# Kernel optimization log

Hardware: AMD Instinct MI355X
Metric: run time of the kernel (lower is better)

## Reference

```python
import jax, jax.numpy as jnp
import numpy as np

INPUT_DIM = 1024
HIDDEN_DIM = 1024


def setup_inputs() -> dict:
    key = jax.random.key(0)
    ks = jax.random.split(key, 7)
    B, S = 4, 2048
    s = 1.0 / np.sqrt(INPUT_DIM)
    x = jax.random.normal(ks[0], (B, S, INPUT_DIM), dtype=jnp.float32)
    Wq = jax.random.normal(ks[1], (HIDDEN_DIM, INPUT_DIM), dtype=jnp.float32) * s
    bq = jnp.zeros((HIDDEN_DIM,), dtype=jnp.float32)
    Wk = jax.random.normal(ks[2], (HIDDEN_DIM, INPUT_DIM), dtype=jnp.float32) * s
    bk = jnp.zeros((HIDDEN_DIM,), dtype=jnp.float32)
    Wv = jax.random.normal(ks[3], (HIDDEN_DIM, INPUT_DIM), dtype=jnp.float32) * s
    bv = jnp.zeros((HIDDEN_DIM,), dtype=jnp.float32)
    return {"x": x, "Wq": Wq, "bq": bq, "Wk": Wk, "bk": bk, "Wv": Wv, "bv": bv}


def reference(x, Wq, bq, Wk, bk, Wv, bv):
    # Linear layers: y = x @ W.T + b (torch nn.Linear convention)
    q = jnp.einsum('bsi,hi->bsh', x, Wq) + bq
    k = jnp.einsum('bsi,hi->bsh', x, Wk) + bk
    v = jnp.einsum('bsi,hi->bsh', x, Wv) + bv
    scale = 1.0 / jnp.sqrt(jnp.asarray(q.shape[-1], dtype=q.dtype))
    scores = jnp.einsum('bsh,bth->bst', q, k) * scale  # [B,S,S]
    attention_weights = jax.nn.softmax(scores, axis=-1)
    weighted_sum = jnp.einsum('bst,bth->bsh', attention_weights, v)
    return (weighted_sum, attention_weights)
```

## Files before the change

kernel.cpp:

```cpp
#include <hip/hip_runtime.h>
#include <hip/hip_bf16.h>
#include <cstdint>


typedef __bf16 bf16x8 __attribute__((ext_vector_type(8)));
typedef float  f32x4  __attribute__((ext_vector_type(4)));

__device__ __forceinline__ void load_lds16(const __bf16* g, __bf16* l) {
    __builtin_amdgcn_global_load_lds(
        (const __attribute__((address_space(1))) void*)g,
        (__attribute__((address_space(3))) void*)l,
        16, 0, 0);
}

__global__ __launch_bounds__(256) void cvt_all(
        const float* __restrict__ x,
        const float* __restrict__ wq, const float* __restrict__ wk,
        const float* __restrict__ wv,
        const float* __restrict__ bq, const float* __restrict__ bk,
        const float* __restrict__ bv,
        __bf16* __restrict__ xb, __bf16* __restrict__ wb,
        float* __restrict__ bias3) {
    const long NX = 1048576, NW = 131072;
    long i = (long)blockIdx.x * 256 + threadIdx.x;
    const float* src; __bf16* dst; long c;
    if (i < NX) { src = x; dst = xb; c = i; }
    else if (i < NX + 3 * NW) {
        long j = i - NX;
        src = (j < NW) ? wq : (j < 2 * NW) ? wk : wv;
        c = j % NW;
        dst = wb + (j / NW) * (NW * 8);
    } else if (i < NX + 3 * NW + 384) {
        long cidx = i - (NX + 3 * NW);
        int seg = (int)(cidx >> 7);
        const float* bs = (seg == 0) ? bq : (seg == 1) ? bk : bv;
        long off = (cidx & 127) * 8;
        float4 a = *(const float4*)(bs + off);
        float4 b = *(const float4*)(bs + off + 4);
        *(float4*)(bias3 + cidx * 8)     = a;
        *(float4*)(bias3 + cidx * 8 + 4) = b;
        return;
    } else return;
    const float4* s4 = (const float4*)src;
    float4 a = s4[2 * c], b = s4[2 * c + 1];
    bf16x8 o;
    o[0] = (__bf16)a.x; o[1] = (__bf16)a.y; o[2] = (__bf16)a.z; o[3] = (__bf16)a.w;
    o[4] = (__bf16)b.x; o[5] = (__bf16)b.y; o[6] = (__bf16)b.z; o[7] = (__bf16)b.w;
    ((bf16x8*)dst)[c] = o;
}

template <int MODE>
__global__ __launch_bounds__(256, 4) void gemm_nt(
        const __bf16* __restrict__ A, const __bf16* __restrict__ Bt,
        void* __restrict__ C0, void* __restrict__ C1, void* __restrict__ C2,
        const float* __restrict__ bias,
        int lda, int ldb, int ldc, long sA, long sB, long sC,
        int K, float scale) {
    __shared__ __bf16 smem[16384];
    __bf16* lA = smem;
    __bf16* lB = smem + 8192;

    const int tid  = threadIdx.x;
    const int lane = tid & 63;
    const int wave = tid >> 6;
    const int mblk = blockIdx.y * 128;
    const int nblk = blockIdx.x * 128;
    const int z    = blockIdx.z;
    A  += (long)z * sA;
    Bt += (long)z * sB;

    const int wm = (wave >> 1) * 64;
    const int wn = (wave & 1) * 64;

    f32x4 zero = {0.f, 0.f, 0.f, 0.f};
    f32x4 acc[4][4];
#pragma unroll
    for (int i = 0; i < 4; ++i)
#pragma unroll
        for (int j = 0; j < 4; ++j) acc[i][j] = zero;

    const int rsel = lane & 15;
    const int quad = lane >> 4;

    int srow[4], scol[4];
#pragma unroll
    for (int it = 0; it < 4; ++it) {
        int s  = tid + it * 256;
        srow[it] = s >> 3;
        scol[it] = ((s & 7) ^ (srow[it] & 7)) * 8;
    }

    for (int k0 = 0; k0 < K; k0 += 64) {
#pragma unroll
        for (int it = 0; it < 4; ++it) {
            int s = tid + it * 256;
            load_lds16(A  + (long)(mblk + srow[it]) * lda + k0 + scol[it], lA + s * 8);
            load_lds16(Bt + (long)(nblk + srow[it]) * ldb + k0 + scol[it], lB + s * 8);
        }
        __syncthreads();

#pragma unroll
        for (int half = 0; half < 2; ++half) {
            const int cq = quad + half * 4;
            bf16x8 fa[4], fb[4];
#pragma unroll
            for (int i = 0; i < 4; ++i) {
                int ra = wm + i * 16 + rsel;
                fa[i] = *(const bf16x8*)&lA[(ra * 8 + (cq ^ (ra & 7))) * 8];
                int rb = wn + i * 16 + rsel;
                fb[i] = *(const bf16x8*)&lB[(rb * 8 + (cq ^ (rb & 7))) * 8];
            }
#pragma unroll
            for (int i = 0; i < 4; ++i)
#pragma unroll
                for (int j = 0; j < 4; ++j)
                    acc[i][j] = __builtin_amdgcn_mfma_f32_16x16x32_bf16(
                        fa[i], fb[j], acc[i][j], 0, 0, 0);
        }
        __syncthreads();
    }

    const int rq = quad * 4;
    if constexpr (MODE == 0) {
        if (nblk >= 2048) {
            __bf16* tbuf = smem;
#pragma unroll
            for (int i = 0; i < 4; ++i) {
#pragma unroll
                for (int j = 0; j < 4; ++j) {
                    const int n_loc = wn + j * 16 + rsel;
                    const float bv = bias[nblk + n_loc];
                    const int m_loc = wm + i * 16 + rq;
                    const int c  = m_loc >> 3;
                    const int cs = c ^ (n_loc & 15);
                    __bf16* dst = &tbuf[n_loc * 128 + cs * 8 + (m_loc & 7)];
                    __bf16 tmp[4];
#pragma unroll
                    for (int r = 0; r < 4; ++r) tmp[r] = (__bf16)(acc[i][j][r] + bv);
                    *(uint64_t*)dst = *(const uint64_t*)tmp;
                }
            }
            __syncthreads();
            {
                __bf16* vt = (__bf16*)C2;
                const int n_loc = tid & 127;
                const int cpart = tid >> 7;
                const long b = mblk >> 11;
                const long t0 = mblk & 2047;
                const long h  = nblk - 2048 + n_loc;
                __bf16* gdst = vt + b * (1024L * 2048) + h * 2048 + t0;
#pragma unroll
                for (int s = 0; s < 8; ++s) {
                    int c  = cpart * 8 + s;
                    int cs = c ^ (n_loc & 15);
                    bf16x8 vchunk = *(const bf16x8*)&tbuf[n_loc * 128 + cs * 8];
                    *(bf16x8*)(gdst + c * 8) = vchunk;
                }
            }
        } else {
#pragma unroll
            for (int i = 0; i < 4; ++i) {
#pragma unroll
                for (int j = 0; j < 4; ++j) {
                    const int n = nblk + wn + j * 16 + rsel;
                    __bf16* C = (n < 1024) ? (__bf16*)C0 : (__bf16*)C1;
                    const int col = n & 1023;
                    float bv = bias[n];
#pragma unroll
                    for (int r = 0; r < 4; ++r) {
                        int m = mblk + wm + i * 16 + rq + r;
                        C[(long)m * ldc + col] = (__bf16)(acc[i][j][r] + bv);
                    }
                }
            }
        }
    } else {
#pragma unroll
        for (int i = 0; i < 4; ++i) {
#pragma unroll
            for (int j = 0; j < 4; ++j) {
                const int n = nblk + wn + j * 16 + rsel;
                float* C = (float*)C0 + (long)z * sC;
                if constexpr (MODE == 1) {
#pragma unroll
                    for (int r = 0; r < 4; ++r) {
                        int m = mblk + wm + i * 16 + rq + r;
                        C[(long)m * ldc + n] = acc[i][j][r] * scale;
                    }
                } else {
#pragma unroll
                    for (int r = 0; r < 4; ++r) {
                        int m = mblk + wm + i * 16 + rq + r;
                        C[(long)m * ldc + n] = acc[i][j][r];
                    }
                }
            }
        }
    }
}

__global__ __launch_bounds__(256) void softmax_rows(
        float* __restrict__ P, __bf16* __restrict__ Pb) {
    const long row = blockIdx.x;
    float*  p  = P  + row * 2048;
    __bf16* pb = Pb + row * 2048;
    const int tid  = threadIdx.x;
    const int lane = tid & 63;
    const int wave = tid >> 6;

    float4 v0 = ((const float4*)p)[tid * 2];
    float4 v1 = ((const float4*)p)[tid * 2 + 1];
    float e[8] = {v0.x, v0.y, v0.z, v0.w, v1.x, v1.y, v1.z, v1.w};

    float mx = e[0];
#pragma unroll
    for (int i = 1; i < 8; ++i) mx = fmaxf(mx, e[i]);
#pragma unroll
    for (int o = 1; o < 64; o <<= 1) mx = fmaxf(mx, __shfl_xor(mx, o, 64));

    __shared__ float redm[4], reds[4];
    if (lane == 0) redm[wave] = mx;
    __syncthreads();
    mx = fmaxf(fmaxf(redm[0], redm[1]), fmaxf(redm[2], redm[3]));

    float sum = 0.f;
#pragma unroll
    for (int i = 0; i < 8; ++i) { e[i] = __expf(e[i] - mx); sum += e[i]; }
#pragma unroll
    for (int o = 1; o < 64; o <<= 1) sum += __shfl_xor(sum, o, 64);
    if (lane == 0) reds[wave] = sum;
    __syncthreads();
    sum = reds[0] + reds[1] + reds[2] + reds[3];
    const float inv = 1.f / sum;

    float4 o0, o1;
    o0.x = e[0] * inv; o0.y = e[1] * inv; o0.z = e[2] * inv; o0.w = e[3] * inv;
    o1.x = e[4] * inv; o1.y = e[5] * inv; o1.z = e[6] * inv; o1.w = e[7] * inv;
    ((float4*)p)[tid * 2]     = o0;
    ((float4*)p)[tid * 2 + 1] = o1;
    bf16x8 ob;
    ob[0] = (__bf16)o0.x; ob[1] = (__bf16)o0.y; ob[2] = (__bf16)o0.z; ob[3] = (__bf16)o0.w;
    ob[4] = (__bf16)o1.x; ob[5] = (__bf16)o1.y; ob[6] = (__bf16)o1.z; ob[7] = (__bf16)o1.w;
    ((bf16x8*)pb)[tid] = ob;
}

extern "C" void kernel_launch(void* const* d_in, const int* in_sizes, int n_in,
                              void* d_out, int out_size, void* d_ws, size_t ws_size,
                              hipStream_t stream) {
    const float* x  = (const float*)d_in[0];
    const float* Wq = (const float*)d_in[1];
    const float* bq = (const float*)d_in[2];
    const float* Wk = (const float*)d_in[3];
    const float* bk = (const float*)d_in[4];
    const float* Wv = (const float*)d_in[5];
    const float* bv = (const float*)d_in[6];

    const int  S = 2048, H = 1024, I = 1024, B = 4;
    const long MS = (long)B * S;
    float* out_ws  = (float*)d_out;
    float* out_att = (float*)d_out + (long)B * S * H;

    char* w = (char*)d_ws;
    __bf16* x_bf   = (__bf16*)w; w += MS * I * 2;
    __bf16* wqkv   = (__bf16*)w; w += (long)3 * H * I * 2;
    float*  bias3  = (float*)w;  w += 4096 * 4;
    __bf16* q_bf   = (__bf16*)w; w += MS * H * 2;
    __bf16* k_bf   = (__bf16*)w; w += MS * H * 2;
    __bf16* vt_bf  = (__bf16*)w; w += MS * H * 2;
    __bf16* p_bf   = (__bf16*)w; w += (long)B * S * S * 2;

    {
        long tot = 1048576 + 3 * 131072 + 384;
        cvt_all<<<dim3((unsigned)((tot + 255) / 256)), dim3(256), 0, stream>>>(
            x, Wq, Wk, Wv, bq, bk, bv, x_bf, wqkv, bias3);
    }

    gemm_nt<0><<<dim3(24, 64, 1), dim3(256), 0, stream>>>(
        x_bf, wqkv, q_bf, k_bf, vt_bf, bias3,
        1024, 1024, 1024, 0, 0, 0, 1024, 1.f);

    gemm_nt<1><<<dim3(16, 16, 4), dim3(256), 0, stream>>>(
        q_bf, k_bf, out_att, nullptr, nullptr, nullptr,
        1024, 1024, 2048, (long)S * H, (long)S * H, (long)S * S, 1024, 0.03125f);

    softmax_rows<<<dim3(8192), dim3(256), 0, stream>>>(out_att, p_bf);

    gemm_nt<2><<<dim3(8, 16, 4), dim3(256), 0, stream>>>(
        p_bf, vt_bf, out_ws, nullptr, nullptr, nullptr,
        2048, 2048, 1024, (long)S * S, (long)S * H, (long)S * H, 2048, 1.f);
}
```

Baseline: 303.6 us.

## Use 256x128 tiles with 8 waves and a triple-buffered async LDS pipeline

The GEMM kernel now uses 512-thread blocks computing 256x128 output tiles. Global-to-LDS loads are issued two k-steps ahead into a three-stage ring buffer, with counted vmcnt waits and raw barriers replacing the two __syncthreads per iteration. MFMA sections are wrapped in setprio. The aim is to hide load latency behind compute and reuse each B tile across more rows. In exchange it uses about 144KB of LDS per block and halves the number of blocks, which may reduce occupancy and cause tail effects.

```diff
diff --git a/kernel.cpp b/kernel.cpp
--- a/kernel.cpp
+++ b/kernel.cpp
@@ -50,27 +50,27 @@
 }
 
 template <int MODE>
-__global__ __launch_bounds__(256, 4) void gemm_nt(
+__global__ __launch_bounds__(512, 2) void gemm_nt8(
         const __bf16* __restrict__ A, const __bf16* __restrict__ Bt,
         void* __restrict__ C0, void* __restrict__ C1, void* __restrict__ C2,
         const float* __restrict__ bias,
         int lda, int ldb, int ldc, long sA, long sB, long sC,
         int K, float scale) {
-    __shared__ __bf16 smem[16384];
-    __bf16* lA = smem;
-    __bf16* lB = smem + 8192;
+    __shared__ __bf16 smem[73728];
 
     const int tid  = threadIdx.x;
     const int lane = tid & 63;
     const int wave = tid >> 6;
-    const int mblk = blockIdx.y * 128;
+    const int mblk = blockIdx.y * 256;
     const int nblk = blockIdx.x * 128;
     const int z    = blockIdx.z;
     A  += (long)z * sA;
     Bt += (long)z * sB;
 
-    const int wm = (wave >> 1) * 64;
-    const int wn = (wave & 1) * 64;
+    const int wmb  = (wave >> 1) * 64;
+    const int wnb  = (wave & 1) * 64;
+    const int rsel = lane & 15;
+    const int quad = lane >> 4;
 
     f32x4 zero = {0.f, 0.f, 0.f, 0.f};
     f32x4 acc[4][4];
@@ -79,61 +79,99 @@
 #pragma unroll
         for (int j = 0; j < 4; ++j) acc[i][j] = zero;
 
-    const int rsel = lane & 15;
-    const int quad = lane >> 4;
-
-    int srow[4], scol[4];
+    int srow[4], scg[4];
 #pragma unroll
     for (int it = 0; it < 4; ++it) {
-        int s  = tid + it * 256;
+        int s = it * 512 + tid;
         srow[it] = s >> 3;
-        scol[it] = ((s & 7) ^ (srow[it] & 7)) * 8;
+        scg[it]  = ((s & 7) ^ (srow[it] & 7)) * 8;
     }
 
-    for (int k0 = 0; k0 < K; k0 += 64) {
-#pragma unroll
-        for (int it = 0; it < 4; ++it) {
-            int s = tid + it * 256;
-            load_lds16(A  + (long)(mblk + srow[it]) * lda + k0 + scol[it], lA + s * 8);
-            load_lds16(Bt + (long)(nblk + srow[it]) * ldb + k0 + scol[it], lB + s * 8);
-        }
-        __syncthreads();
-
-#pragma unroll
-        for (int half = 0; half < 2; ++half) {
-            const int cq = quad + half * 4;
-            bf16x8 fa[4], fb[4];
-#pragma unroll
-            for (int i = 0; i < 4; ++i) {
-                int ra = wm + i * 16 + rsel;
-                fa[i] = *(const bf16x8*)&lA[(ra * 8 + (cq ^ (ra & 7))) * 8];
-                int rb = wn + i * 16 + rsel;
-                fb[i] = *(const bf16x8*)&lB[(rb * 8 + (cq ^ (rb & 7))) * 8];
-            }
-#pragma unroll
-            for (int i = 0; i < 4; ++i)
-#pragma unroll
-                for (int j = 0; j < 4; ++j)
-                    acc[i][j] = __builtin_amdgcn_mfma_f32_16x16x32_bf16(
-                        fa[i], fb[j], acc[i][j], 0, 0, 0);
-        }
-        __syncthreads();
+    auto STAGE = [&](int t, int bufb) {
+        const long k0 = (long)t << 6;
+        __bf16* lAb = smem + bufb * 24576;
+        __bf16* lBb = lAb + 16384;
+#pragma unroll
+        for (int it = 0; it < 4; ++it)
+            load_lds16(A + (long)(mblk + srow[it]) * lda + k0 + scg[it],
+                       lAb + (it * 512 + tid) * 8);
+#pragma unroll
+        for (int it = 0; it < 2; ++it)
+            load_lds16(Bt + (long)(nblk + srow[it]) * ldb + k0 + scg[it],
+                       lBb + (it * 512 + tid) * 8);
+    };
+
+    const int NT = K >> 6;
+
+    STAGE(0, 0);
+    STAGE(1, 1);
+    asm volatile("s_waitcnt vmcnt(6)" ::: "memory");
+    __builtin_amdgcn_s_barrier();
+    __builtin_amdgcn_sched_barrier(0);
+
+    int cur = 0;
+    for (int t = 0; t < NT; ++t) {
+        __bf16* lA = smem + cur * 24576;
+        __bf16* lB = lA + 16384;
+
+        bf16x8 fa0[4], fa1[4], fb0[4], fb1[4];
+#pragma unroll
+        for (int i = 0; i < 4; ++i) {
+            const int ra = wmb + i * 16 + rsel;
+            const int rx = ra * 8, sw = ra & 7;
+            fa0[i] = *(const bf16x8*)&lA[(rx + (quad ^ sw)) * 8];
+            fa1[i] = *(const bf16x8*)&lA[(rx + ((quad + 4) ^ sw)) * 8];
+        }
+#pragma unroll
+        for (int j = 0; j < 4; ++j) {
+            const int rb = wnb + j * 16 + rsel;
+            const int rx = rb * 8, sw = rb & 7;
+            fb0[j] = *(const bf16x8*)&lB[(rx + (quad ^ sw)) * 8];
+            fb1[j] = *(const bf16x8*)&lB[(rx + ((quad + 4) ^ sw)) * 8];
+        }
+
+        int nxt = cur + 2; if (nxt >= 3) nxt -= 3;
+        if (t + 2 < NT) STAGE(t + 2, nxt);
+
+        __builtin_amdgcn_s_setprio(1);
+#pragma unroll
+        for (int i = 0; i < 4; ++i)
+#pragma unroll
+            for (int j = 0; j < 4; ++j)
+                acc[i][j] = __builtin_amdgcn_mfma_f32_16x16x32_bf16(
+                    fa0[i], fb0[j], acc[i][j], 0, 0, 0);
+#pragma unroll
+        for (int i = 0; i < 4; ++i)
+#pragma unroll
+            for (int j = 0; j < 4; ++j)
+                acc[i][j] = __builtin_amdgcn_mfma_f32_16x16x32_bf16(
+                    fa1[i], fb1[j], acc[i][j], 0, 0, 0);
+        __builtin_amdgcn_s_setprio(0);
+
+        if (t + 1 < NT) {
+            if (t + 2 < NT) asm volatile("s_waitcnt vmcnt(6)" ::: "memory");
+            else            asm volatile("s_waitcnt vmcnt(0)" ::: "memory");
+            __builtin_amdgcn_s_barrier();
+            __builtin_amdgcn_sched_barrier(0);
+        }
+        cur += 1; if (cur == 3) cur = 0;
     }
 
     const int rq = quad * 4;
     if constexpr (MODE == 0) {
         if (nblk >= 2048) {
+            __syncthreads();
             __bf16* tbuf = smem;
 #pragma unroll
             for (int i = 0; i < 4; ++i) {
 #pragma unroll
                 for (int j = 0; j < 4; ++j) {
-                    const int n_loc = wn + j * 16 + rsel;
+                    const int n_loc = wnb + j * 16 + rsel;
                     const float bv = bias[nblk + n_loc];
-                    const int m_loc = wm + i * 16 + rq;
+                    const int m_loc = wmb + i * 16 + rq;
                     const int c  = m_loc >> 3;
-                    const int cs = c ^ (n_loc & 15);
-                    __bf16* dst = &tbuf[n_loc * 128 + cs * 8 + (m_loc & 7)];
+                    const int cs = c ^ (n_loc & 31);
+                    __bf16* dst = &tbuf[n_loc * 256 + cs * 8 + (m_loc & 7)];
                     __bf16 tmp[4];
 #pragma unroll
                     for (int r = 0; r < 4; ++r) tmp[r] = (__bf16)(acc[i][j][r] + bv);
@@ -142,19 +180,17 @@
             }
             __syncthreads();
             {
-                __bf16* vt = (__bf16*)C2;
-                const int n_loc = tid & 127;
-                const int cpart = tid >> 7;
-                const long b = mblk >> 11;
+                const long b  = mblk >> 11;
                 const long t0 = mblk & 2047;
-                const long h  = nblk - 2048 + n_loc;
-                __bf16* gdst = vt + b * (1024L * 2048) + h * 2048 + t0;
-#pragma unroll
-                for (int s = 0; s < 8; ++s) {
-                    int c  = cpart * 8 + s;
-                    int cs = c ^ (n_loc & 15);
-                    bf16x8 vchunk = *(const bf16x8*)&tbuf[n_loc * 128 + cs * 8];
-                    *(bf16x8*)(gdst + c * 8) = vchunk;
+                const long hbase = nblk - 2048;
+                __bf16* vt = (__bf16*)C2 + b * (2048L * 1024) + t0;
+#pragma unroll
+                for (int pass = 0; pass < 8; ++pass) {
+                    int h_loc = pass * 16 + wave * 2 + (lane >> 5);
+                    int c  = lane & 31;
+                    int cs = c ^ (h_loc & 31);
+                    bf16x8 vchunk = *(const bf16x8*)&tbuf[h_loc * 256 + cs * 8];
+                    *(bf16x8*)(vt + (hbase + h_loc) * 2048 + c * 8) = vchunk;
                 }
             }
         } else {
@@ -162,37 +198,32 @@
             for (int i = 0; i < 4; ++i) {
 #pragma unroll
                 for (int j = 0; j < 4; ++j) {
-                    const int n = nblk + wn + j * 16 + rsel;
+                    const int n = nblk + wnb + j * 16 + rsel;
                     __bf16* C = (n < 1024) ? (__bf16*)C0 : (__bf16*)C1;
                     const int col = n & 1023;
                     float bv = bias[n];
 #pragma unroll
                     for (int r = 0; r < 4; ++r) {
-                        int m = mblk + wm + i * 16 + rq + r;
+                        int m = mblk + wmb + i * 16 + rq + r;
                         C[(long)m * ldc + col] = (__bf16)(acc[i][j][r] + bv);
                     }
                 }
             }
         }
     } else {
+        float* C = (float*)C0 + (long)z * sC;
 #pragma unroll
         for (int i = 0; i < 4; ++i) {
 #pragma unroll
             for (int j = 0; j < 4; ++j) {
-                const int n = nblk + wn + j * 16 + rsel;
-                float* C = (float*)C0 + (long)z * sC;
-                if constexpr (MODE == 1) {
-#pragma unroll
-                    for (int r = 0; r < 4; ++r) {
-                        int m = mblk + wm + i * 16 + rq + r;
+                const int n = nblk + wnb + j * 16 + rsel;
+#pragma unroll
+                for (int r = 0; r < 4; ++r) {
+                    int m = mblk + wmb + i * 16 + rq + r;
+                    if constexpr (MODE == 1)
                         C[(long)m * ldc + n] = acc[i][j][r] * scale;
-                    }
-                } else {
-#pragma unroll
-                    for (int r = 0; r < 4; ++r) {
-                        int m = mblk + wm + i * 16 + rq + r;
+                    else
                         C[(long)m * ldc + n] = acc[i][j][r];
-                    }
                 }
             }
         }
@@ -275,17 +306,17 @@
             x, Wq, Wk, Wv, bq, bk, bv, x_bf, wqkv, bias3);
     }
 
-    gemm_nt<0><<<dim3(24, 64, 1), dim3(256), 0, stream>>>(
+    gemm_nt8<0><<<dim3(24, 32, 1), dim3(512), 0, stream>>>(
         x_bf, wqkv, q_bf, k_bf, vt_bf, bias3,
         1024, 1024, 1024, 0, 0, 0, 1024, 1.f);
 
-    gemm_nt<1><<<dim3(16, 16, 4), dim3(256), 0, stream>>>(
+    gemm_nt8<1><<<dim3(16, 8, 4), dim3(512), 0, stream>>>(
         q_bf, k_bf, out_att, nullptr, nullptr, nullptr,
         1024, 1024, 2048, (long)S * H, (long)S * H, (long)S * S, 1024, 0.03125f);
 
     softmax_rows<<<dim3(8192), dim3(256), 0, stream>>>(out_att, p_bf);
 
-    gemm_nt<2><<<dim3(8, 16, 4), dim3(256), 0, stream>>>(
+    gemm_nt8<2><<<dim3(8, 8, 4), dim3(512), 0, stream>>>(
         p_bf, vt_bf, out_ws, nullptr, nullptr, nullptr,
         2048, 2048, 1024, (long)S * S, (long)S * H, (long)S * H, 2048, 1.f);
 }
```

New measurement: 309.6 us. Within noise of the previous version (+2.0%).

## Add 256x256 eight-wave double-buffered GEMM with phased prefetch for QKV and scores

Applied to the files above, without the earlier changes.

Adds a new GEMM kernel with 256x256 tiles, 512 threads and double-buffered LDS (128 KB). It splits each K step into four MFMA phases, issuing the global-to-LDS prefetch for the next tiles between phases under barriers and priority hints. This kernel now runs the QKV projection and the QK^T score GEMM, while the PV GEMM keeps the old kernel under a new name. The aim is to raise reuse per loaded byte and hide load latency behind MFMA work. The cost is fewer blocks (occupancy drops to one block per CU given the LDS size) and tail effects on the small score grid of 256 blocks.

```diff
diff --git a/kernel.cpp b/kernel.cpp
--- a/kernel.cpp
+++ b/kernel.cpp
@@ -12,6 +12,28 @@
         (__attribute__((address_space(3))) void*)l,
         16, 0, 0);
 }
+
+#define PH_MID() do {                                       \
+    __builtin_amdgcn_sched_barrier(0);                      \
+    __builtin_amdgcn_s_barrier();                           \
+    asm volatile("s_waitcnt lgkmcnt(0)" ::: "memory");      \
+    __builtin_amdgcn_sched_barrier(0);                      \
+    __builtin_amdgcn_s_setprio(1);                          \
+} while (0)
+
+#define PH_END() do {                                       \
+    __builtin_amdgcn_s_setprio(0);                          \
+    __builtin_amdgcn_s_barrier();                           \
+    __builtin_amdgcn_sched_barrier(0);                      \
+} while (0)
+
+#define PH_END_VM(cond) do {                                \
+    __builtin_amdgcn_s_setprio(0);                          \
+    if (cond) asm volatile("s_waitcnt vmcnt(6)" ::: "memory"); \
+    else      asm volatile("s_waitcnt vmcnt(0)" ::: "memory"); \
+    __builtin_amdgcn_s_barrier();                           \
+    __builtin_amdgcn_sched_barrier(0);                      \
+} while (0)
 
 __global__ __launch_bounds__(256) void cvt_all(
         const float* __restrict__ x,
@@ -50,12 +72,220 @@
 }
 
 template <int MODE>
-__global__ __launch_bounds__(256, 4) void gemm_nt(
+__global__ __launch_bounds__(512, 2) void gemm8p(
         const __bf16* __restrict__ A, const __bf16* __restrict__ Bt,
         void* __restrict__ C0, void* __restrict__ C1, void* __restrict__ C2,
         const float* __restrict__ bias,
         int lda, int ldb, int ldc, long sA, long sB, long sC,
         int K, float scale) {
+    __shared__ __bf16 smem[65536];
+
+    const int tid  = threadIdx.x;
+    const int lane = tid & 63;
+    const int wave = tid >> 6;
+    const int mblk = blockIdx.y * 256;
+    const int nblk = blockIdx.x * 256;
+    const int z    = blockIdx.z;
+    A  += (long)z * sA;
+    Bt += (long)z * sB;
+
+    const int wm   = (wave >> 2) * 128;
+    const int wn   = (wave & 3) * 64;
+    const int rsel = lane & 15;
+    const int quad = lane >> 4;
+    const int arow = wm + rsel;
+    const int brow = wn + rsel;
+
+    f32x4 zero = {0.f, 0.f, 0.f, 0.f};
+    f32x4 acc[8][4];
+#pragma unroll
+    for (int i = 0; i < 8; ++i)
+#pragma unroll
+        for (int j = 0; j < 4; ++j) acc[i][j] = zero;
+
+    long offA[2], offB[2]; int loff[2];
+#pragma unroll
+    for (int it = 0; it < 2; ++it) {
+        int s = it * 512 + tid;
+        int r = s >> 3, sl = s & 7;
+        int cg = sl ^ (r & 7);
+        offA[it] = (long)(mblk + r) * lda + cg * 8;
+        offB[it] = (long)(nblk + r) * ldb + cg * 8;
+        loff[it] = s * 8;
+    }
+
+    auto stage_half = [&](int isB, int h, int t) {
+        const __bf16* G = isB ? Bt : A;
+        const int ld = isB ? ldb : lda;
+        const long hoff = (long)h * 128 * ld;
+        const long k0 = (long)t << 6;
+        __bf16* dstb = smem + (t & 1) * 32768 + isB * 16384 + h * 8192;
+#pragma unroll
+        for (int it = 0; it < 2; ++it)
+            load_lds16(G + (isB ? offB[it] : offA[it]) + hoff + k0,
+                       dstb + loff[it]);
+    };
+
+    auto ld_frag = [&](const __bf16* base, int row, int q) -> bf16x8 {
+        return *(const bf16x8*)&base[(row * 8 + (q ^ (row & 7))) * 8];
+    };
+
+    const int NT = K >> 6;
+
+    stage_half(1, 0, 0); stage_half(1, 1, 0);
+    stage_half(0, 0, 0); stage_half(0, 1, 0);
+    stage_half(1, 0, 1); stage_half(1, 1, 1); stage_half(0, 0, 1);
+    asm volatile("s_waitcnt vmcnt(6)" ::: "memory");
+    __builtin_amdgcn_s_barrier();
+    __builtin_amdgcn_sched_barrier(0);
+
+    for (int tt = 0; tt < NT; tt += 2) {
+#pragma unroll
+        for (int sub = 0; sub < 2; ++sub) {
+            const int t = tt + sub;
+            const __bf16* lA = smem + sub * 32768;
+            const __bf16* lB = lA + 16384;
+            bf16x8 faL[4][2], faH[4][2], fb[4][2];
+
+#pragma unroll
+            for (int j = 0; j < 4; ++j)
+#pragma unroll
+                for (int k = 0; k < 2; ++k)
+                    fb[j][k] = ld_frag(lB, brow + j * 16, k * 4 + quad);
+#pragma unroll
+            for (int i = 0; i < 4; ++i)
+#pragma unroll
+                for (int k = 0; k < 2; ++k)
+                    faL[i][k] = ld_frag(lA, arow + i * 16, k * 4 + quad);
+            if (t + 1 < NT) stage_half(0, 1, t + 1);
+            PH_MID();
+#pragma unroll
+            for (int i = 0; i < 4; ++i)
+#pragma unroll
+                for (int j = 0; j < 2; ++j)
+#pragma unroll
+                    for (int k = 0; k < 2; ++k)
+                        acc[i][j] = __builtin_amdgcn_mfma_f32_16x16x32_bf16(
+                            faL[i][k], fb[j][k], acc[i][j], 0, 0, 0);
+            PH_END();
+
+#pragma unroll
+            for (int i = 0; i < 4; ++i)
+#pragma unroll
+                for (int k = 0; k < 2; ++k)
+                    faH[i][k] = ld_frag(lA, arow + 64 + i * 16, k * 4 + quad);
+            if (t + 2 < NT) stage_half(1, 0, t + 2);
+            PH_MID();
+#pragma unroll
+            for (int i = 0; i < 4; ++i)
+#pragma unroll
+                for (int j = 0; j < 2; ++j)
+#pragma unroll
+                    for (int k = 0; k < 2; ++k)
+                        acc[4 + i][j] = __builtin_amdgcn_mfma_f32_16x16x32_bf16(
+                            faH[i][k], fb[j][k], acc[4 + i][j], 0, 0, 0);
+            PH_END();
+
+            if (t + 2 < NT) stage_half(1, 1, t + 2);
+            PH_MID();
+#pragma unroll
+            for (int i = 0; i < 4; ++i)
+#pragma unroll
+                for (int j = 0; j < 2; ++j)
+#pragma unroll
+                    for (int k = 0; k < 2; ++k)
+                        acc[i][2 + j] = __builtin_amdgcn_mfma_f32_16x16x32_bf16(
+                            faL[i][k], fb[2 + j][k], acc[i][2 + j], 0, 0, 0);
+            PH_END();
+
+            if (t + 2 < NT) stage_half(0, 0, t + 2);
+            PH_MID();
+#pragma unroll
+            for (int i = 0; i < 4; ++i)
+#pragma unroll
+                for (int j = 0; j < 2; ++j)
+#pragma unroll
+                    for (int k = 0; k < 2; ++k)
+                        acc[4 + i][2 + j] = __builtin_amdgcn_mfma_f32_16x16x32_bf16(
+                            faH[i][k], fb[2 + j][k], acc[4 + i][2 + j], 0, 0, 0);
+            PH_END_VM(t + 2 < NT);
+        }
+    }
+
+    const int rq = quad * 4;
+    if constexpr (MODE == 0) {
+        if (nblk >= 2048) {
+            __syncthreads();
+            __bf16* tbuf = smem;
+#pragma unroll
+            for (int i = 0; i < 8; ++i) {
+#pragma unroll
+                for (int j = 0; j < 4; ++j) {
+                    const int n_loc = wn + j * 16 + rsel;
+                    const float bv = bias[nblk + n_loc];
+                    const int m_loc = wm + i * 16 + rq;
+                    const int c  = m_loc >> 3;
+                    const int cs = c ^ (n_loc & 31);
+                    __bf16* dst = &tbuf[n_loc * 256 + cs * 8 + (m_loc & 7)];
+                    __bf16 tmp[4];
+#pragma unroll
+                    for (int r = 0; r < 4; ++r) tmp[r] = (__bf16)(acc[i][j][r] + bv);
+                    *(uint64_t*)dst = *(const uint64_t*)tmp;
+                }
+            }
+            __syncthreads();
+            {
+                const long b  = mblk >> 11;
+                const long t0 = mblk & 2047;
+                const long hbase = nblk - 2048;
+                __bf16* vt = (__bf16*)C2 + b * (1024L * 2048) + t0;
+#pragma unroll
+                for (int pass = 0; pass < 16; ++pass) {
+                    int h_loc = pass * 16 + (tid >> 5);
+                    int c  = tid & 31;
+                    int cs = c ^ (h_loc & 31);
+                    bf16x8 vchunk = *(const bf16x8*)&tbuf[h_loc * 256 + cs * 8];
+                    *(bf16x8*)(vt + (hbase + h_loc) * 2048 + c * 8) = vchunk;
+                }
+            }
+        } else {
+#pragma unroll
+            for (int i = 0; i < 8; ++i) {
+#pragma unroll
+                for (int j = 0; j < 4; ++j) {
+                    const int n = nblk + wn + j * 16 + rsel;
+                    __bf16* C = (n < 1024) ? (__bf16*)C0 : (__bf16*)C1;
+                    const int col = n & 1023;
+                    float bv = bias[n];
+#pragma unroll
+                    for (int r = 0; r < 4; ++r) {
+                        int m = mblk + wm + i * 16 + rq + r;
+                        C[(long)m * ldc + col] = (__bf16)(acc[i][j][r] + bv);
+                    }
+                }
+            }
+        }
+    } else {
+        float* C = (float*)C0 + (long)z * sC;
+#pragma unroll
+        for (int i = 0; i < 8; ++i) {
+#pragma unroll
+            for (int j = 0; j < 4; ++j) {
+                const int n = nblk + wn + j * 16 + rsel;
+#pragma unroll
+                for (int r = 0; r < 4; ++r) {
+                    int m = mblk + wm + i * 16 + rq + r;
+                    C[(long)m * ldc + n] = acc[i][j][r] * scale;
+                }
+            }
+        }
+    }
+}
+
+__global__ __launch_bounds__(256, 4) void gemm_pv(
+        const __bf16* __restrict__ A, const __bf16* __restrict__ Bt,
+        float* __restrict__ C,
+        int lda, int ldb, int ldc, long sA, long sB, long sC, int K) {
     __shared__ __bf16 smem[16384];
     __bf16* lA = smem;
     __bf16* lB = smem + 8192;
@@ -102,98 +332,35 @@
 #pragma unroll
         for (int half = 0; half < 2; ++half) {
             const int cq = quad + half * 4;
-            bf16x8 fa[4], fb[4];
+            bf16x8 fa[4], fbv[4];
 #pragma unroll
             for (int i = 0; i < 4; ++i) {
                 int ra = wm + i * 16 + rsel;
                 fa[i] = *(const bf16x8*)&lA[(ra * 8 + (cq ^ (ra & 7))) * 8];
                 int rb = wn + i * 16 + rsel;
-                fb[i] = *(const bf16x8*)&lB[(rb * 8 + (cq ^ (rb & 7))) * 8];
+                fbv[i] = *(const bf16x8*)&lB[(rb * 8 + (cq ^ (rb & 7))) * 8];
             }
 #pragma unroll
             for (int i = 0; i < 4; ++i)
 #pragma unroll
                 for (int j = 0; j < 4; ++j)
                     acc[i][j] = __builtin_amdgcn_mfma_f32_16x16x32_bf16(
-                        fa[i], fb[j], acc[i][j], 0, 0, 0);
+                        fa[i], fbv[j], acc[i][j], 0, 0, 0);
         }
         __syncthreads();
     }
 
     const int rq = quad * 4;
-    if constexpr (MODE == 0) {
-        if (nblk >= 2048) {
-            __bf16* tbuf = smem;
-#pragma unroll
-            for (int i = 0; i < 4; ++i) {
-#pragma unroll
-                for (int j = 0; j < 4; ++j) {
-                    const int n_loc = wn + j * 16 + rsel;
-                    const float bv = bias[nblk + n_loc];
-                    const int m_loc = wm + i * 16 + rq;
-                    const int c  = m_loc >> 3;
-                    const int cs = c ^ (n_loc & 15);
-                    __bf16* dst = &tbuf[n_loc * 128 + cs * 8 + (m_loc & 7)];
-                    __bf16 tmp[4];
-#pragma unroll
-                    for (int r = 0; r < 4; ++r) tmp[r] = (__bf16)(acc[i][j][r] + bv);
-                    *(uint64_t*)dst = *(const uint64_t*)tmp;
-                }
-            }
-            __syncthreads();
-            {
-                __bf16* vt = (__bf16*)C2;
-                const int n_loc = tid & 127;
-                const int cpart = tid >> 7;
-                const long b = mblk >> 11;
-                const long t0 = mblk & 2047;
-                const long h  = nblk - 2048 + n_loc;
-                __bf16* gdst = vt + b * (1024L * 2048) + h * 2048 + t0;
-#pragma unroll
-                for (int s = 0; s < 8; ++s) {
-                    int c  = cpart * 8 + s;
-                    int cs = c ^ (n_loc & 15);
-                    bf16x8 vchunk = *(const bf16x8*)&tbuf[n_loc * 128 + cs * 8];
-                    *(bf16x8*)(gdst + c * 8) = vchunk;
-                }
-            }
-        } else {
-#pragma unroll
-            for (int i = 0; i < 4; ++i) {
-#pragma unroll
-                for (int j = 0; j < 4; ++j) {
-                    const int n = nblk + wn + j * 16 + rsel;
-                    __bf16* C = (n < 1024) ? (__bf16*)C0 : (__bf16*)C1;
-                    const int col = n & 1023;
-                    float bv = bias[n];
-#pragma unroll
-                    for (int r = 0; r < 4; ++r) {
-                        int m = mblk + wm + i * 16 + rq + r;
-                        C[(long)m * ldc + col] = (__bf16)(acc[i][j][r] + bv);
-                    }
-                }
-            }
-        }
-    } else {
-#pragma unroll
-        for (int i = 0; i < 4; ++i) {
-#pragma unroll
-            for (int j = 0; j < 4; ++j) {
-                const int n = nblk + wn + j * 16 + rsel;
-                float* C = (float*)C0 + (long)z * sC;
-                if constexpr (MODE == 1) {
-#pragma unroll
-                    for (int r = 0; r < 4; ++r) {
-                        int m = mblk + wm + i * 16 + rq + r;
-                        C[(long)m * ldc + n] = acc[i][j][r] * scale;
-                    }
-                } else {
-#pragma unroll
-                    for (int r = 0; r < 4; ++r) {
-                        int m = mblk + wm + i * 16 + rq + r;
-                        C[(long)m * ldc + n] = acc[i][j][r];
-                    }
-                }
+#pragma unroll
+    for (int i = 0; i < 4; ++i) {
+#pragma unroll
+        for (int j = 0; j < 4; ++j) {
+            const int n = nblk + wn + j * 16 + rsel;
+            float* Cz = C + (long)z * sC;
+#pragma unroll
+            for (int r = 0; r < 4; ++r) {
+                int m = mblk + wm + i * 16 + rq + r;
+                Cz[(long)m * ldc + n] = acc[i][j][r];
             }
         }
     }
@@ -275,17 +442,17 @@
             x, Wq, Wk, Wv, bq, bk, bv, x_bf, wqkv, bias3);
     }
 
-    gemm_nt<0><<<dim3(24, 64, 1), dim3(256), 0, stream>>>(
+    gemm8p<0><<<dim3(12, 32, 1), dim3(512), 0, stream>>>(
         x_bf, wqkv, q_bf, k_bf, vt_bf, bias3,
         1024, 1024, 1024, 0, 0, 0, 1024, 1.f);
 
-    gemm_nt<1><<<dim3(16, 16, 4), dim3(256), 0, stream>>>(
+    gemm8p<1><<<dim3(8, 8, 4), dim3(512), 0, stream>>>(
         q_bf, k_bf, out_att, nullptr, nullptr, nullptr,
         1024, 1024, 2048, (long)S * H, (long)S * H, (long)S * S, 1024, 0.03125f);
 
     softmax_rows<<<dim3(8192), dim3(256), 0, stream>>>(out_att, p_bf);
 
-    gemm_nt<2><<<dim3(8, 16, 4), dim3(256), 0, stream>>>(
-        p_bf, vt_bf, out_ws, nullptr, nullptr, nullptr,
-        2048, 2048, 1024, (long)S * S, (long)S * H, (long)S * H, 2048, 1.f);
-}
+    gemm_pv<<<dim3(8, 16, 4), dim3(256), 0, stream>>>(
+        p_bf, vt_bf, out_ws,
+        2048, 2048, 1024, (long)S * S, (long)S * H, (long)S * H, 2048);
+}
```

New measurement: 309.5 us. No clear change (+1.9%).
